# Kernel tuning notes

Hardware: AMD Instinct MI355X
Metric: run time of the kernel (lower is better)

The kernel has to match this reference:

```python
import jax, jax.numpy as jnp
import numpy as np


def channel_attention(x):
    # Faithful to torch: proj_key = x.view(B, -1, C) is a memory RESHAPE, not a transpose.
    B, C, H, W = x.shape
    N = H * W
    pq = x.reshape(B, C, N)          # [B, C, N]
    pk = x.reshape(B, N, C)          # [B, N, C] -- reshape, NOT pq transposed
    attn = jax.nn.softmax(jnp.einsum('bcn,bnd->bcd', pq, pk), axis=-1)  # [B, C, C]
    out = jnp.einsum('bcd,bdn->bcn', attn, pq).reshape(B, C, H, W)
    return out + x


def positional_attention(x):
    B, C, H, W = x.shape
    N = H * W
    pk = x.reshape(B, C, N)                                  # [B, C, N]
    # proj_query = pk transposed -> attn[b, n, m] over spatial positions
    attn = jax.nn.softmax(jnp.einsum('bcn,bcm->bnm', pk, pk), axis=-1)  # [B, N, N]
    # out = bmm(pk, attn^T): out[b, c, m] = sum_n pk[b, c, n] * attn[b, m, n]
    out = jnp.einsum('bcn,bmn->bcm', pk, attn).reshape(B, C, H, W)
    return out + x


def setup_inputs() -> dict:
    key = jax.random.key(0)
    x = jax.random.normal(key, (4, 512, 64, 64), dtype=jnp.float32)
    return {"x": x}


def reference(x):
    x_ca = channel_attention(x)
    x_pa = positional_attention(x_ca)
    return x_pa
```

## Files before the change

kernel.cpp:

```cpp
#include <hip/hip_runtime.h>

#define BATCH 4
#define CH 512
#define NSP 4096

typedef __attribute__((ext_vector_type(8))) short bfrag8;
typedef __attribute__((ext_vector_type(4))) float f32x4;
typedef unsigned short u16;

#define AS1 __attribute__((address_space(1)))
#define AS3 __attribute__((address_space(3)))
__device__ __forceinline__ void gload16(const void* g, void* l) {
    __builtin_amdgcn_global_load_lds((const AS1 void*)g, (AS3 void*)l, 16, 0, 0);
}

__device__ __forceinline__ void split_bf16(float y, u16& h, u16& l) {
    unsigned int u = __float_as_uint(y);
    h = (u16)(u >> 16);
    float r = y - __uint_as_float(((unsigned int)h) << 16);
    l = (u16)(__float_as_uint(r) >> 16);
}
__device__ __forceinline__ float join_bf16(u16 h, u16 l) {
    return __uint_as_float(((unsigned int)h) << 16) + __uint_as_float(((unsigned int)l) << 16);
}

__global__ __launch_bounds__(256) void k_prep_cn(const float* __restrict__ X,
                                                 u16* __restrict__ XHi,
                                                 u16* __restrict__ XLo,
                                                 u16* __restrict__ XT1hi,
                                                 u16* __restrict__ XT1lo) {
    __shared__ unsigned int t[64][65];
    const size_t boff = (size_t)blockIdx.z * CH * NSP;
    const int c0 = blockIdx.y * 64, n0 = blockIdx.x * 64;
    const int r = threadIdx.x >> 4, col4 = (threadIdx.x & 15) * 4;
#pragma unroll
    for (int it = 0; it < 4; it++) {
        int rl = r + it * 16;
        float4 v = *(const float4*)(X + boff + (size_t)(c0 + rl) * NSP + n0 + col4);
        ushort4 h, l;
        split_bf16(v.x, h.x, l.x);
        split_bf16(v.y, h.y, l.y);
        split_bf16(v.z, h.z, l.z);
        split_bf16(v.w, h.w, l.w);
        *(ushort4*)(XHi + boff + (size_t)(c0 + rl) * NSP + n0 + col4) = h;
        *(ushort4*)(XLo + boff + (size_t)(c0 + rl) * NSP + n0 + col4) = l;
        t[rl][col4 + 0] = ((unsigned int)h.x << 16) | l.x;
        t[rl][col4 + 1] = ((unsigned int)h.y << 16) | l.y;
        t[rl][col4 + 2] = ((unsigned int)h.z << 16) | l.z;
        t[rl][col4 + 3] = ((unsigned int)h.w << 16) | l.w;
    }
    __syncthreads();
#pragma unroll
    for (int it = 0; it < 4; it++) {
        int cl = r + it * 16;
        unsigned int p0 = t[col4 + 0][cl];
        unsigned int p1 = t[col4 + 1][cl];
        unsigned int p2 = t[col4 + 2][cl];
        unsigned int p3 = t[col4 + 3][cl];
        ushort4 hv, lv;
        hv.x = p0 >> 16; hv.y = p1 >> 16; hv.z = p2 >> 16; hv.w = p3 >> 16;
        lv.x = p0 & 0xffff; lv.y = p1 & 0xffff; lv.z = p2 & 0xffff; lv.w = p3 & 0xffff;
        *(ushort4*)(XT1hi + boff + (size_t)(n0 + cl) * CH + c0 + col4) = hv;
        *(ushort4*)(XT1lo + boff + (size_t)(n0 + cl) * CH + c0 + col4) = lv;
    }
}

__global__ __launch_bounds__(256) void k_prep_nc(const float* __restrict__ X,
                                                 u16* __restrict__ XT2hi,
                                                 u16* __restrict__ XT2lo) {
    __shared__ unsigned int t[64][65];
    const size_t boff = (size_t)blockIdx.z * CH * NSP;
    const int n0 = blockIdx.x * 64, d0 = blockIdx.y * 64;
    const int r = threadIdx.x >> 4, col4 = (threadIdx.x & 15) * 4;
#pragma unroll
    for (int it = 0; it < 4; it++) {
        int rl = r + it * 16;
        float4 v = *(const float4*)(X + boff + (size_t)(n0 + rl) * CH + d0 + col4);
        ushort4 h, l;
        split_bf16(v.x, h.x, l.x);
        split_bf16(v.y, h.y, l.y);
        split_bf16(v.z, h.z, l.z);
        split_bf16(v.w, h.w, l.w);
        t[rl][col4 + 0] = ((unsigned int)h.x << 16) | l.x;
        t[rl][col4 + 1] = ((unsigned int)h.y << 16) | l.y;
        t[rl][col4 + 2] = ((unsigned int)h.z << 16) | l.z;
        t[rl][col4 + 3] = ((unsigned int)h.w << 16) | l.w;
    }
    __syncthreads();
#pragma unroll
    for (int it = 0; it < 4; it++) {
        int cl = r + it * 16;
        unsigned int p0 = t[col4 + 0][cl];
        unsigned int p1 = t[col4 + 1][cl];
        unsigned int p2 = t[col4 + 2][cl];
        unsigned int p3 = t[col4 + 3][cl];
        ushort4 hv, lv;
        hv.x = p0 >> 16; hv.y = p1 >> 16; hv.z = p2 >> 16; hv.w = p3 >> 16;
        lv.x = p0 & 0xffff; lv.y = p1 & 0xffff; lv.z = p2 & 0xffff; lv.w = p3 & 0xffff;
        *(ushort4*)(XT2hi + boff + (size_t)(d0 + cl) * NSP + n0 + col4) = hv;
        *(ushort4*)(XT2lo + boff + (size_t)(d0 + cl) * NSP + n0 + col4) = lv;
    }
}

__global__ __launch_bounds__(256, 2) void k1_mfma(const u16* __restrict__ XHi,
                                                  const u16* __restrict__ XLo,
                                                  const u16* __restrict__ XT2hi,
                                                  const u16* __restrict__ XT2lo,
                                                  float* __restrict__ Pk) {
    __shared__ __align__(16) char smem[32768];
    char* Ahi = smem;
    char* Alo = smem + 8192;
    char* Bhi = smem + 16384;
    char* Blo = smem + 24576;
    const int bid = blockIdx.x;
    const int xcd = bid & 7;
    const int i1 = bid >> 3;
    const int group = xcd * 4 + (i1 >> 4);
    const int b = group >> 3, kz = group & 7;
    const int tile = i1 & 15;
    const int c0 = (tile >> 2) * 128, d0 = (tile & 3) * 128;
    const size_t boff = (size_t)b * CH * NSP;
    const int tid = threadIdx.x, lane = tid & 63, w = tid >> 6;
    const int wr = w >> 1, wc = w & 1;
    const int rl = lane >> 2;
    const int cb = (lane & 3) * 8;
    f32x4 acc[4][4];
#pragma unroll
    for (int i = 0; i < 4; i++)
#pragma unroll
        for (int j = 0; j < 4; j++) acc[i][j] = (f32x4){0.f, 0.f, 0.f, 0.f};

    const int kbeg = kz * 512, kend = kbeg + 512;
    for (int k0 = kbeg; k0 < kend; k0 += 32) {
#pragma unroll
        for (int s = 0; s < 2; s++) {
            int idx = w * 2 + s;
            int row = 16 * idx + rl;
            gload16(XHi + boff + (size_t)(c0 + row) * NSP + k0 + cb, Ahi + idx * 1024);
            gload16(XLo + boff + (size_t)(c0 + row) * NSP + k0 + cb, Alo + idx * 1024);
            gload16(XT2hi + boff + (size_t)(d0 + row) * NSP + k0 + cb, Bhi + idx * 1024);
            gload16(XT2lo + boff + (size_t)(d0 + row) * NSP + k0 + cb, Blo + idx * 1024);
        }
        __syncthreads();
        bfrag8 ah[4], al[4], bh[4], bl[4];
        const int q16 = (lane >> 4) * 16;
        const int l15 = (lane & 15);
#pragma unroll
        for (int i = 0; i < 4; i++) {
            int offa = (wr * 64 + i * 16 + l15) * 64 + q16;
            ah[i] = *(const bfrag8*)(Ahi + offa);
            al[i] = *(const bfrag8*)(Alo + offa);
            int offb = (wc * 64 + i * 16 + l15) * 64 + q16;
            bh[i] = *(const bfrag8*)(Bhi + offb);
            bl[i] = *(const bfrag8*)(Blo + offb);
        }
#pragma unroll
        for (int i = 0; i < 4; i++)
#pragma unroll
            for (int j = 0; j < 4; j++) {
                acc[i][j] = __builtin_amdgcn_mfma_f32_16x16x32_bf16(ah[i], bh[j], acc[i][j], 0, 0, 0);
                acc[i][j] = __builtin_amdgcn_mfma_f32_16x16x32_bf16(ah[i], bl[j], acc[i][j], 0, 0, 0);
                acc[i][j] = __builtin_amdgcn_mfma_f32_16x16x32_bf16(al[i], bh[j], acc[i][j], 0, 0, 0);
            }
        __syncthreads();
    }
    float* Lb = Pk + (size_t)kz * BATCH * CH * CH + (size_t)b * CH * CH;
    const int col = lane & 15, qr = (lane >> 4) * 4;
#pragma unroll
    for (int i = 0; i < 4; i++)
#pragma unroll
        for (int j = 0; j < 4; j++)
#pragma unroll
            for (int r = 0; r < 4; r++)
                Lb[(size_t)(c0 + wr * 64 + 16 * i + qr + r) * CH + d0 + wc * 64 + 16 * j + col] =
                    acc[i][j][r];
}

__global__ __launch_bounds__(256) void k_combine8(const float* __restrict__ Pk,
                                                  float* __restrict__ Lg) {
    const size_t MM = (size_t)BATCH * CH * CH;
    size_t i = ((size_t)blockIdx.x * 256 + threadIdx.x) * 4;
    float4 s = *(const float4*)(Pk + i);
#pragma unroll
    for (int z = 1; z < 8; z++) {
        float4 v = *(const float4*)(Pk + z * MM + i);
        s.x += v.x; s.y += v.y; s.z += v.z; s.w += v.w;
    }
    *(float4*)(Lg + i) = s;
}

__global__ __launch_bounds__(256) void k_softmax_pack512(float* __restrict__ Lg) {
    __shared__ float buf[512];
    __shared__ float red[256];
    const int tid = threadIdx.x;
    float* row = Lg + (size_t)blockIdx.x * 512;
    float2 v = *(const float2*)(row + tid * 2);
    buf[tid * 2] = v.x;
    buf[tid * 2 + 1] = v.y;
    red[tid] = fmaxf(v.x, v.y);
    __syncthreads();
    for (int s = 128; s > 0; s >>= 1) {
        if (tid < s) red[tid] = fmaxf(red[tid], red[tid + s]);
        __syncthreads();
    }
    float m = red[0];
    __syncthreads();
    float e0 = __expf(buf[tid * 2] - m), e1 = __expf(buf[tid * 2 + 1] - m);
    buf[tid * 2] = e0;
    buf[tid * 2 + 1] = e1;
    red[tid] = e0 + e1;
    __syncthreads();
    for (int s = 128; s > 0; s >>= 1) {
        if (tid < s) red[tid] += red[tid + s];
        __syncthreads();
    }
    float inv = 1.0f / red[0];
    u16* u = (u16*)row;
    u16 h0, l0, h1, l1;
    split_bf16(buf[tid * 2] * inv, h0, l0);
    split_bf16(buf[tid * 2 + 1] * inv, h1, l1);
    __syncthreads();
    u[tid * 2] = h0;
    u[tid * 2 + 1] = h1;
    u[512 + tid * 2] = l0;
    u[512 + tid * 2 + 1] = l1;
}

__global__ __launch_bounds__(256, 2) void k3_mfma(const u16* __restrict__ Lu,
                                                  const u16* __restrict__ XT1hi,
                                                  const u16* __restrict__ XT1lo,
                                                  const float* __restrict__ X,
                                                  u16* __restrict__ Yhi,
                                                  u16* __restrict__ Ylo,
                                                  u16* __restrict__ YThi,
                                                  u16* __restrict__ YTlo) {
    __shared__ __align__(16) char smem[33280];
    char* Ahi = smem;
    char* Alo = smem + 8192;
    char* Bhi = smem + 16384;
    char* Blo = smem + 24576;
    const int b = blockIdx.z;
    const u16* Au = Lu + (size_t)b * CH * 1024;
    const size_t boff = (size_t)b * CH * NSP;
    const float* Xb = X + boff;
    const int tid = threadIdx.x, lane = tid & 63, w = tid >> 6;
    const int wr = w >> 1, wc = w & 1;
    const int c0 = blockIdx.y * 128, n0 = blockIdx.x * 128;
    const int rl = lane >> 2;
    const int cb = (lane & 3) * 8;
    f32x4 acc[4][4];
#pragma unroll
    for (int i = 0; i < 4; i++)
#pragma unroll
        for (int j = 0; j < 4; j++) acc[i][j] = (f32x4){0.f, 0.f, 0.f, 0.f};

    for (int k0 = 0; k0 < CH; k0 += 32) {
#pragma unroll
        for (int s = 0; s < 2; s++) {
            int idx = w * 2 + s;
            int row = 16 * idx + rl;
            gload16(Au + (size_t)(c0 + row) * 1024 + k0 + cb, Ahi + idx * 1024);
            gload16(Au + (size_t)(c0 + row) * 1024 + 512 + k0 + cb, Alo + idx * 1024);
            gload16(XT1hi + boff + (size_t)(n0 + row) * CH + k0 + cb, Bhi + idx * 1024);
            gload16(XT1lo + boff + (size_t)(n0 + row) * CH + k0 + cb, Blo + idx * 1024);
        }
        __syncthreads();
        bfrag8 ah[4], al[4], bh[4], bl[4];
        const int q16 = (lane >> 4) * 16;
        const int l15 = (lane & 15);
#pragma unroll
        for (int i = 0; i < 4; i++) {
            int offa = (wr * 64 + i * 16 + l15) * 64 + q16;
            ah[i] = *(const bfrag8*)(Ahi + offa);
            al[i] = *(const bfrag8*)(Alo + offa);
            int offb = (wc * 64 + i * 16 + l15) * 64 + q16;
            bh[i] = *(const bfrag8*)(Bhi + offb);
            bl[i] = *(const bfrag8*)(Blo + offb);
        }
#pragma unroll
        for (int i = 0; i < 4; i++)
#pragma unroll
            for (int j = 0; j < 4; j++) {
                acc[i][j] = __builtin_amdgcn_mfma_f32_16x16x32_bf16(ah[i], bh[j], acc[i][j], 0, 0, 0);
                acc[i][j] = __builtin_amdgcn_mfma_f32_16x16x32_bf16(ah[i], bl[j], acc[i][j], 0, 0, 0);
                acc[i][j] = __builtin_amdgcn_mfma_f32_16x16x32_bf16(al[i], bh[j], acc[i][j], 0, 0, 0);
            }
        __syncthreads();
    }
    u16* Yhb = Yhi + boff;
    u16* Ylb = Ylo + boff;
    u16* YThb = YThi + boff;
    u16* YTlb = YTlo + boff;
    const int col = lane & 15, qr = (lane >> 4) * 4;
    unsigned int* Tb = (unsigned int*)smem;
#pragma unroll
    for (int round = 0; round < 2; round++) {
        if (wr == round) {
            unsigned int* T = Tb + wc * 4160;
#pragma unroll
            for (int i = 0; i < 4; i++)
#pragma unroll
                for (int j = 0; j < 4; j++)
#pragma unroll
                    for (int r = 0; r < 4; r++) {
                        int cl = 16 * i + qr + r;
                        int nl = 16 * j + col;
                        int c = c0 + wr * 64 + cl;
                        int n = n0 + wc * 64 + nl;
                        float v = acc[i][j][r] + Xb[(size_t)c * NSP + n];
                        u16 h, l;
                        split_bf16(v, h, l);
                        Yhb[(size_t)c * NSP + n] = h;
                        Ylb[(size_t)c * NSP + n] = l;
                        T[nl * 65 + cl] = ((unsigned int)h << 16) | l;
                    }
        }
        __syncthreads();
        if (wr == round) {
            unsigned int* T = Tb + wc * 4160;
            const int cl = (lane & 15) * 4;
#pragma unroll
            for (int rep = 0; rep < 16; rep++) {
                int nq = rep * 4 + (lane >> 4);
                unsigned int p0 = T[nq * 65 + cl];
                unsigned int p1 = T[nq * 65 + cl + 1];
                unsigned int p2 = T[nq * 65 + cl + 2];
                unsigned int p3 = T[nq * 65 + cl + 3];
                ushort4 hv, lv;
                hv.x = p0 >> 16; hv.y = p1 >> 16; hv.z = p2 >> 16; hv.w = p3 >> 16;
                lv.x = p0 & 0xffff; lv.y = p1 & 0xffff; lv.z = p2 & 0xffff; lv.w = p3 & 0xffff;
                size_t o = (size_t)(n0 + wc * 64 + nq) * CH + c0 + wr * 64 + cl;
                *(ushort4*)(YThb + o) = hv;
                *(ushort4*)(YTlb + o) = lv;
            }
        }
        __syncthreads();
    }
}

__global__ __launch_bounds__(512, 2) void k4_mfma(const u16* __restrict__ YThi0,
                                                  const u16* __restrict__ YTlo0,
                                                  float* __restrict__ S0) {
    __shared__ __align__(16) char smem[131072];
    const int tid = threadIdx.x, lane = tid & 63, w = tid >> 6;
    const int wr = w >> 2, wc = w & 3;
    const int bid = blockIdx.x;
    const int swz = (bid & 7) * 64 + (bid >> 3);
    const int rb = swz >> 8;
    const int tl = swz & 255;
    const int n0 = (tl >> 4) * 256, m0 = (tl & 15) * 256;
    const u16* Phi = YThi0 + (size_t)rb * NSP * CH;
    const u16* Plo = YTlo0 + (size_t)rb * NSP * CH;
    float* S = S0 + (size_t)rb * NSP * NSP;

    const int rl = lane >> 2;
    const int cb = (((lane & 3) ^ ((lane >> 3) & 3)) * 8);
    const int l15 = lane & 15;
    const int q16 = (((lane >> 4) ^ ((lane >> 1) & 3)) * 16);

    auto STAGE = [&](const u16* mat, int r0, int kt, int u) {
        char* dst = smem + (kt & 1) * 65536 + u * 16384;
        const int k0 = kt * 32;
#pragma unroll
        for (int s = 0; s < 2; s++) {
            int idx = w * 2 + s;
            gload16(mat + (size_t)(r0 + idx * 16 + rl) * CH + k0 + cb, dst + idx * 1024);
        }
    };

    f32x4 acc[8][4];
#pragma unroll
    for (int i = 0; i < 8; i++)
#pragma unroll
        for (int j = 0; j < 4; j++) acc[i][j] = (f32x4){0.f, 0.f, 0.f, 0.f};
    bfrag8 ah[8], al[8], bh[4], bl[4];

    auto LDA = [&](const char* base, bfrag8* a) {
#pragma unroll
        for (int i = 0; i < 8; i++)
            a[i] = *(const bfrag8*)(base + (wr * 128 + i * 16 + l15) * 64 + q16);
    };
    auto LDB = [&](const char* base, bfrag8* bv) {
#pragma unroll
        for (int j = 0; j < 4; j++)
            bv[j] = *(const bfrag8*)(base + (wc * 64 + j * 16 + l15) * 64 + q16);
    };
    auto MMA = [&](const bfrag8* a, const bfrag8* bv) {
        __builtin_amdgcn_s_setprio(1);
#pragma unroll
        for (int i = 0; i < 8; i++)
#pragma unroll
            for (int j = 0; j < 4; j++)
                acc[i][j] = __builtin_amdgcn_mfma_f32_16x16x32_bf16(a[i], bv[j], acc[i][j], 0, 0, 0);
        __builtin_amdgcn_s_setprio(0);
        __builtin_amdgcn_s_barrier();
        __builtin_amdgcn_sched_barrier(0);
    };

#define WAITB(N)                                          \
    asm volatile("s_waitcnt vmcnt(" #N ")" ::: "memory"); \
    __builtin_amdgcn_s_barrier();

    STAGE(Phi, n0, 0, 0);
    STAGE(Phi, m0, 0, 2);
    STAGE(Plo, n0, 0, 1);
    STAGE(Plo, m0, 0, 3);
    STAGE(Phi, n0, 1, 0);
    STAGE(Phi, m0, 1, 2);
    STAGE(Plo, n0, 1, 1);
    WAITB(10)

    for (int t = 0; t < 14; ++t) {
        const char* buf = smem + (t & 1) * 65536;
        LDA(buf, ah);
        LDB(buf + 32768, bh);
        STAGE(Plo, m0, t + 1, 3);
        WAITB(10)
        MMA(ah, bh);
        LDA(buf + 16384, al);
        STAGE(Phi, n0, t + 2, 0);
        STAGE(Phi, m0, t + 2, 2);
        WAITB(12)
        MMA(al, bh);
        LDB(buf + 49152, bl);
        STAGE(Plo, n0, t + 2, 1);
        WAITB(10)
        MMA(ah, bl);
    }
    {
        const char* buf = smem;
        LDA(buf, ah);
        LDB(buf + 32768, bh);
        STAGE(Plo, m0, 15, 3);
        WAITB(10)
        MMA(ah, bh);
        LDA(buf + 16384, al);
        WAITB(8)
        MMA(al, bh);
        LDB(buf + 49152, bl);
        WAITB(4)
        MMA(ah, bl);
    }
    {
        const char* buf = smem + 65536;
        LDA(buf, ah);
        LDB(buf + 32768, bh);
        WAITB(2)
        MMA(ah, bh);
        LDA(buf + 16384, al);
        WAITB(0)
        MMA(al, bh);
        LDB(buf + 49152, bl);
        __builtin_amdgcn_s_barrier();
        MMA(ah, bl);
    }
#undef WAITB

    const int col = lane & 15, qr = (lane >> 4) * 4;
#pragma unroll
    for (int i = 0; i < 8; i++)
#pragma unroll
        for (int j = 0; j < 4; j++)
#pragma unroll
            for (int r = 0; r < 4; r++)
                S[(size_t)(n0 + wr * 128 + 16 * i + qr + r) * NSP + m0 + wc * 64 + 16 * j + col] =
                    acc[i][j][r];
}

__global__ __launch_bounds__(256) void k_softmax_pack(float* __restrict__ S) {
    __shared__ float buf[4096];
    __shared__ float red[256];
    const int tid = threadIdx.x;
    float* row = S + (size_t)blockIdx.x * NSP;
    float m = -INFINITY;
#pragma unroll
    for (int it = 0; it < 4; it++) {
        int i = (tid + it * 256) * 4;
        float4 v = *(const float4*)(row + i);
        buf[i] = v.x; buf[i + 1] = v.y; buf[i + 2] = v.z; buf[i + 3] = v.w;
        m = fmaxf(m, fmaxf(fmaxf(v.x, v.y), fmaxf(v.z, v.w)));
    }
    red[tid] = m;
    __syncthreads();
    for (int s = 128; s > 0; s >>= 1) {
        if (tid < s) red[tid] = fmaxf(red[tid], red[tid + s]);
        __syncthreads();
    }
    m = red[0];
    __syncthreads();
    float sum = 0.f;
#pragma unroll
    for (int it = 0; it < 4; it++) {
        int i = (tid + it * 256) * 4;
        float e0 = __expf(buf[i] - m), e1 = __expf(buf[i + 1] - m);
        float e2 = __expf(buf[i + 2] - m), e3 = __expf(buf[i + 3] - m);
        buf[i] = e0; buf[i + 1] = e1; buf[i + 2] = e2; buf[i + 3] = e3;
        sum += e0 + e1 + e2 + e3;
    }
    red[tid] = sum;
    __syncthreads();
    for (int s = 128; s > 0; s >>= 1) {
        if (tid < s) red[tid] += red[tid + s];
        __syncthreads();
    }
    float inv = 1.0f / red[0];
    u16* u = (u16*)row;
#pragma unroll
    for (int it = 0; it < 4; it++) {
        int i = (tid + it * 256) * 4;
        ushort4 hv;
        hv.x = (u16)(__float_as_uint(buf[i] * inv) >> 16);
        hv.y = (u16)(__float_as_uint(buf[i + 1] * inv) >> 16);
        hv.z = (u16)(__float_as_uint(buf[i + 2] * inv) >> 16);
        hv.w = (u16)(__float_as_uint(buf[i + 3] * inv) >> 16);
        *(ushort4*)(u + i) = hv;
    }
}

__global__ __launch_bounds__(256, 2) void k6_mfma(const u16* __restrict__ Yhi0,
                                                  const u16* __restrict__ Ylo0,
                                                  const u16* __restrict__ Su,
                                                  float* __restrict__ Out0,
                                                  float* __restrict__ Pp0,
                                                  float* __restrict__ Pp1) {
    __shared__ __align__(16) char smem[16384];
    char* Ahi = smem;
    char* Bhi = smem + 8192;
    const int tid = threadIdx.x, lane = tid & 63, w = tid >> 6;
    const int wr = w >> 1, wc = w & 1;
    const int m0 = blockIdx.x * 128, c0 = blockIdx.y * 128;
    const int rb = blockIdx.z >> 1, kz = blockIdx.z & 1;
    const u16* Yhi = Yhi0 + (size_t)rb * CH * NSP;
    const u16* Ylo = Ylo0 + (size_t)rb * CH * NSP;
    const u16* Pu = Su + (size_t)rb * NSP * NSP * 2;
    float* Out = Out0 + (size_t)rb * CH * NSP;
    float* Ppart = rb ? Pp1 : Pp0;
    const int kb = kz * 2048;
    const int rl = lane >> 2;
    const int cb = (lane & 3) * 8;
    f32x4 acc[4][4];
#pragma unroll
    for (int i = 0; i < 4; i++)
#pragma unroll
        for (int j = 0; j < 4; j++) acc[i][j] = (f32x4){0.f, 0.f, 0.f, 0.f};

    for (int k0 = 0; k0 < 2048; k0 += 32) {
        const int kk = kb + k0;
#pragma unroll
        for (int s = 0; s < 2; s++) {
            int idx = w * 2 + s;
            int row = 16 * idx + rl;
            gload16(Yhi + (size_t)(c0 + row) * NSP + kk + cb, Ahi + idx * 1024);
            gload16(Pu + (size_t)(m0 + row) * 8192 + kk + cb, Bhi + idx * 1024);
        }
        __syncthreads();
        bfrag8 ah[4], bh[4];
        const int q16 = (lane >> 4) * 16;
        const int l15 = (lane & 15);
#pragma unroll
        for (int i = 0; i < 4; i++) {
            ah[i] = *(const bfrag8*)(Ahi + (wr * 64 + i * 16 + l15) * 64 + q16);
            bh[i] = *(const bfrag8*)(Bhi + (wc * 64 + i * 16 + l15) * 64 + q16);
        }
#pragma unroll
        for (int i = 0; i < 4; i++)
#pragma unroll
            for (int j = 0; j < 4; j++)
                acc[i][j] = __builtin_amdgcn_mfma_f32_16x16x32_bf16(ah[i], bh[j], acc[i][j], 0, 0, 0);
        __syncthreads();
    }
    const int col = lane & 15, qr = (lane >> 4) * 4;
    if (kz == 0) {
#pragma unroll
        for (int i = 0; i < 4; i++)
#pragma unroll
            for (int j = 0; j < 4; j++)
#pragma unroll
                for (int r = 0; r < 4; r++) {
                    int c = c0 + wr * 64 + 16 * i + qr + r;
                    int mm = m0 + wc * 64 + 16 * j + col;
                    Out[(size_t)c * NSP + mm] =
                        acc[i][j][r] +
                        join_bf16(Yhi[(size_t)c * NSP + mm], Ylo[(size_t)c * NSP + mm]);
                }
    } else {
#pragma unroll
        for (int i = 0; i < 4; i++)
#pragma unroll
            for (int j = 0; j < 4; j++)
#pragma unroll
                for (int r = 0; r < 4; r++) {
                    int c = c0 + wr * 64 + 16 * i + qr + r;
                    int mm = m0 + wc * 64 + 16 * j + col;
                    Ppart[(size_t)c * NSP + mm] = acc[i][j][r];
                }
    }
}

__global__ __launch_bounds__(256) void k_fixup(float* __restrict__ Out0,
                                               const float* __restrict__ Pp0,
                                               const float* __restrict__ Pp1) {
    const size_t CN = (size_t)CH * NSP;
    const int b = blockIdx.y;
    const float* P = b ? Pp1 : Pp0;
    float* O = Out0 + (size_t)b * CN;
    size_t i = ((size_t)blockIdx.x * 256 + threadIdx.x) * 4;
    float4 o = *(const float4*)(O + i);
    float4 a = *(const float4*)(P + i);
    o.x += a.x; o.y += a.y; o.z += a.z; o.w += a.w;
    *(float4*)(O + i) = o;
}

extern "C" void kernel_launch(void* const* d_in, const int* in_sizes, int n_in,
                              void* d_out, int out_size, void* d_ws, size_t ws_size,
                              hipStream_t stream) {
    const float* x = (const float*)d_in[0];
    float* out = (float*)d_out;

    char* p = (char*)d_ws;
    const size_t SZ16 = (size_t)BATCH * CH * NSP * 2;
    const size_t HALF = SZ16 / 2;
    u16* XHi = (u16*)p;
    u16* XLo = (u16*)(p + SZ16);
    u16* XT2hi = (u16*)(p + 2 * SZ16);
    u16* XT2lo = (u16*)(p + 3 * SZ16);
    u16* XT1hi = (u16*)(p + 4 * SZ16);
    u16* XT1lo = (u16*)(p + 5 * SZ16);
    float* S = (float*)p;
    u16* Yhi = (u16*)(p + 8 * SZ16);
    u16* Ylo = (u16*)(p + 9 * SZ16);
    u16* YThi = (u16*)(p + 10 * SZ16);
    u16* YTlo = (u16*)(p + 11 * SZ16);
    float* Pk = (float*)(p + 8 * SZ16);
    float* Lg = (float*)(p + 12 * SZ16);

    k_prep_cn<<<dim3(NSP / 64, CH / 64, BATCH), 256, 0, stream>>>(x, XHi, XLo, XT1hi, XT1lo);
    k_prep_nc<<<dim3(NSP / 64, CH / 64, BATCH), 256, 0, stream>>>(x, XT2hi, XT2lo);
    k1_mfma<<<dim3(512), 256, 0, stream>>>(XHi, XLo, XT2hi, XT2lo, Pk);
    k_combine8<<<dim3((BATCH * CH * CH) / (4 * 256)), 256, 0, stream>>>(Pk, Lg);
    k_softmax_pack512<<<dim3(BATCH * CH), 256, 0, stream>>>(Lg);
    k3_mfma<<<dim3(NSP / 128, CH / 128, BATCH), 256, 0, stream>>>((const u16*)Lg, XT1hi, XT1lo, x,
                                                                  Yhi, Ylo, YThi, YTlo);

    for (int round = 0; round < 2; round++) {
        const size_t b0 = (size_t)(2 * round);
        float* Pp0 = (float*)((char*)YThi + round * HALF);
        float* Pp1 = (float*)((char*)YTlo + round * HALF);
        k4_mfma<<<dim3(512), 512, 0, stream>>>(YThi + b0 * NSP * CH, YTlo + b0 * NSP * CH, S);
        k_softmax_pack<<<dim3(2 * NSP), 256, 0, stream>>>(S);
        k6_mfma<<<dim3(NSP / 128, CH / 128, 4), 256, 0, stream>>>(Yhi + b0 * CH * NSP,
                                                                  Ylo + b0 * CH * NSP,
                                                                  (const u16*)S,
                                                                  out + b0 * CH * NSP, Pp0, Pp1);
        k_fixup<<<dim3((CH * NSP) / (4 * 256), 2), 256, 0, stream>>>(out + b0 * CH * NSP, Pp0, Pp1);
    }
}
```

Baseline: 531.8 us.

## Triple-buffer k6 GEMM with 256-wide tiles, swizzled LDS and async prefetch

Restructures the k6 attention-times-values GEMM. Blocks grow to 512 threads and a 128x256 output tile. Global-to-LDS loads now go through a three-slot ring buffer, prefetching two k-steps ahead with explicit vmcnt waits and raw s_barrier instead of __syncthreads. LDS rows use an XOR swizzle to avoid bank conflicts, and s_setprio raises wave priority around the MFMA bursts. The aim is to hide global load latency and to raise reuse of each staged tile. In exchange it uses 72KB of LDS per block, which limits occupancy, and halves the number of blocks in the grid.

```diff
diff --git a/kernel.cpp b/kernel.cpp
--- a/kernel.cpp
+++ b/kernel.cpp
@@ -517,18 +517,16 @@
     }
 }
 
-__global__ __launch_bounds__(256, 2) void k6_mfma(const u16* __restrict__ Yhi0,
+__global__ __launch_bounds__(512, 2) void k6_mfma(const u16* __restrict__ Yhi0,
                                                   const u16* __restrict__ Ylo0,
                                                   const u16* __restrict__ Su,
                                                   float* __restrict__ Out0,
                                                   float* __restrict__ Pp0,
                                                   float* __restrict__ Pp1) {
-    __shared__ __align__(16) char smem[16384];
-    char* Ahi = smem;
-    char* Bhi = smem + 8192;
+    __shared__ __align__(16) char smem[73728];
     const int tid = threadIdx.x, lane = tid & 63, w = tid >> 6;
-    const int wr = w >> 1, wc = w & 1;
-    const int m0 = blockIdx.x * 128, c0 = blockIdx.y * 128;
+    const int wr = w >> 2, wc = w & 3;
+    const int m0 = blockIdx.x * 256, c0 = blockIdx.y * 128;
     const int rb = blockIdx.z >> 1, kz = blockIdx.z & 1;
     const u16* Yhi = Yhi0 + (size_t)rb * CH * NSP;
     const u16* Ylo = Ylo0 + (size_t)rb * CH * NSP;
@@ -537,38 +535,65 @@
     float* Ppart = rb ? Pp1 : Pp0;
     const int kb = kz * 2048;
     const int rl = lane >> 2;
-    const int cb = (lane & 3) * 8;
-    f32x4 acc[4][4];
-#pragma unroll
-    for (int i = 0; i < 4; i++)
-#pragma unroll
-        for (int j = 0; j < 4; j++) acc[i][j] = (f32x4){0.f, 0.f, 0.f, 0.f};
-
-    for (int k0 = 0; k0 < 2048; k0 += 32) {
-        const int kk = kb + k0;
+    const int cb = (((lane & 3) ^ ((lane >> 3) & 3)) * 8);
+    const int l15 = lane & 15;
+    const int q16 = (((lane >> 4) ^ ((lane >> 1) & 3)) * 16);
+
+    auto STAGE = [&](int kt, int slot) {
+        char* dst = smem + slot * 24576;
+        const int k0 = kb + kt * 32;
+        gload16(Yhi + (size_t)(c0 + w * 16 + rl) * NSP + k0 + cb, dst + w * 1024);
 #pragma unroll
         for (int s = 0; s < 2; s++) {
             int idx = w * 2 + s;
-            int row = 16 * idx + rl;
-            gload16(Yhi + (size_t)(c0 + row) * NSP + kk + cb, Ahi + idx * 1024);
-            gload16(Pu + (size_t)(m0 + row) * 8192 + kk + cb, Bhi + idx * 1024);
-        }
-        __syncthreads();
-        bfrag8 ah[4], bh[4];
-        const int q16 = (lane >> 4) * 16;
-        const int l15 = (lane & 15);
-#pragma unroll
-        for (int i = 0; i < 4; i++) {
-            ah[i] = *(const bfrag8*)(Ahi + (wr * 64 + i * 16 + l15) * 64 + q16);
-            bh[i] = *(const bfrag8*)(Bhi + (wc * 64 + i * 16 + l15) * 64 + q16);
-        }
-#pragma unroll
-        for (int i = 0; i < 4; i++)
-#pragma unroll
-            for (int j = 0; j < 4; j++)
-                acc[i][j] = __builtin_amdgcn_mfma_f32_16x16x32_bf16(ah[i], bh[j], acc[i][j], 0, 0, 0);
-        __syncthreads();
-    }
+            gload16(Pu + (size_t)(m0 + idx * 16 + rl) * 8192 + k0 + cb,
+                    dst + 8192 + idx * 1024);
+        }
+    };
+
+    f32x4 acc[4][4];
+#pragma unroll
+    for (int i = 0; i < 4; i++)
+#pragma unroll
+        for (int j = 0; j < 4; j++) acc[i][j] = (f32x4){0.f, 0.f, 0.f, 0.f};
+    bfrag8 ah[4], bh[4];
+
+#define K6PHASE(SLOT, STSLOT, T, DOSTAGE, WN)                                            \
+    {                                                                                    \
+        const char* bA = smem + (SLOT)*24576;                                            \
+        const char* bB = bA + 8192;                                                      \
+        _Pragma("unroll") for (int i = 0; i < 4; i++) ah[i] =                            \
+            *(const bfrag8*)(bA + (wr * 64 + i * 16 + l15) * 64 + q16);                  \
+        _Pragma("unroll") for (int j = 0; j < 4; j++) bh[j] =                            \
+            *(const bfrag8*)(bB + (wc * 64 + j * 16 + l15) * 64 + q16);                  \
+        if (DOSTAGE) STAGE((T) + 2, (STSLOT));                                           \
+        asm volatile("s_waitcnt vmcnt(" #WN ")" ::: "memory");                           \
+        __builtin_amdgcn_s_barrier();                                                    \
+        __builtin_amdgcn_s_setprio(1);                                                   \
+        _Pragma("unroll") for (int i = 0; i < 4; i++)                                    \
+            _Pragma("unroll") for (int j = 0; j < 4; j++) acc[i][j] =                    \
+                __builtin_amdgcn_mfma_f32_16x16x32_bf16(ah[i], bh[j], acc[i][j], 0, 0, 0); \
+        __builtin_amdgcn_s_setprio(0);                                                   \
+        __builtin_amdgcn_s_barrier();                                                    \
+        __builtin_amdgcn_sched_barrier(0);                                               \
+    }
+
+    STAGE(0, 0);
+    STAGE(1, 1);
+    asm volatile("s_waitcnt vmcnt(3)" ::: "memory");
+    __builtin_amdgcn_s_barrier();
+
+    for (int tt = 0; tt < 60; tt += 3) {
+        K6PHASE(0, 2, tt, true, 3)
+        K6PHASE(1, 0, tt + 1, true, 3)
+        K6PHASE(2, 1, tt + 2, true, 3)
+    }
+    K6PHASE(0, 2, 60, true, 3)
+    K6PHASE(1, 0, 61, true, 3)
+    K6PHASE(2, 0, 62, false, 0)
+    K6PHASE(0, 0, 63, false, 0)
+#undef K6PHASE
+
     const int col = lane & 15, qr = (lane >> 4) * 4;
     if (kz == 0) {
 #pragma unroll
@@ -648,7 +673,7 @@
         float* Pp1 = (float*)((char*)YTlo + round * HALF);
         k4_mfma<<<dim3(512), 512, 0, stream>>>(YThi + b0 * NSP * CH, YTlo + b0 * NSP * CH, S);
         k_softmax_pack<<<dim3(2 * NSP), 256, 0, stream>>>(S);
-        k6_mfma<<<dim3(NSP / 128, CH / 128, 4), 256, 0, stream>>>(Yhi + b0 * CH * NSP,
+        k6_mfma<<<dim3(NSP / 256, CH / 128, 4), 512, 0, stream>>>(Yhi + b0 * CH * NSP,
                                                                   Ylo + b0 * CH * NSP,
                                                                   (const u16*)S,
                                                                   out + b0 * CH * NSP, Pp0, Pp1);
```

After: 528.5 us. About the same (-0.6%).
